# Kernel optimization log

Measured on AMD Instinct MI355X. Metric: run time of the kernel, lower is better.

The kernel has to match this reference:

```python
import jax, jax.numpy as jnp
import numpy as np

BIG = 1.0e6  # sentinel 'infinite' 1D distance (BIG**2 = 1e12 is safely finite in fp32)


def _edt_sq(zero_mask):
    """Exact squared Euclidean distance transform to nearest True in zero_mask.

    Two-pass separable exact EDT (matches scipy.ndimage.distance_transform_edt):
      pass 1: 1-D distance along W via forward/backward cummax scans
      pass 2: min-plus over H: D2[i,j] = min_k g2[k,j] + (i-k)^2
    zero_mask: [H, W] bool (True where the source array equals 0).
    """
    H, W = zero_mask.shape
    col = jnp.arange(W, dtype=jnp.float32)
    # index of last zero to the left / first zero to the right
    last = jax.lax.cummax(jnp.where(zero_mask, col, -BIG), axis=1)
    nxt = -jax.lax.cummax(jnp.where(zero_mask, -col, -BIG), axis=1, reverse=True)
    g = jnp.minimum(jnp.minimum(col - last, nxt - col), BIG)  # [H, W] 1-D dist
    g2 = g * g
    row = jnp.arange(H, dtype=jnp.float32)
    sq = (row[:, None] - row[None, :]) ** 2  # [H, H]
    # D2[i, j] = min_k g2[k, j] + (i - k)^2  -- exact 2-D squared EDT
    return jnp.min(g2[None, :, :] + sq[:, :, None], axis=1)


def _distance_map(mask):
    """Signed distance map: EDT(mask) - EDT(1 - mask); zeros if mask empty."""
    pos = jnp.sqrt(_edt_sq(mask == 0))   # dist of foreground px to nearest background
    neg = jnp.sqrt(_edt_sq(mask != 0))   # dist of background px to nearest foreground
    d = pos - neg
    return jnp.where(mask.sum() == 0, jnp.zeros_like(d), d)


def boundary_loss(pred, target):
    B, C, H, W = pred.shape
    masks = target.reshape(B * C, H, W)
    # sequence over B*C to keep the [H,H,W] min-plus intermediate per-image
    dmaps = jax.lax.map(_distance_map, masks).reshape(B, C, H, W)
    # sum_c mean_{b,h,w}(sig(pred_c)*d_c) / C  ==  overall mean
    return jnp.mean(jax.nn.sigmoid(pred) * dmaps)


def setup_inputs() -> dict:
    key = jax.random.key(0)
    k1, k2 = jax.random.split(key)
    pred = jax.random.normal(k1, (8, 3, 256, 256), dtype=jnp.float32)
    target = jax.random.randint(k2, (8, 3, 256, 256), 0, 2, dtype=jnp.int32)
    return {"pred": pred, "target": target}


def reference(pred, target):
    return boundary_loss(pred, target)
```

## Files before the change

### kernel.cpp

```cpp
#include <hip/hip_runtime.h>
#include <math.h>

#define NIMG 24
#define H    256
#define W    256
#define NPIX (H * W)
#define NROWS (NIMG * H)
#define CPB  16
#define NBLK2 (NIMG * (W / CPB))
#define LDP2 17
#define BIGI 1000000
#define CAPS 1024

__global__ __launch_bounds__(256)
void edt_rows_kernel(const int* __restrict__ tgt,
                     short* __restrict__ f,
                     float* __restrict__ out) {
    if (blockIdx.x == 0 && threadIdx.x == 0) out[0] = 0.0f;

    const int lane = threadIdx.x & 63;
    const int wid  = threadIdx.x >> 6;
    const int gw   = blockIdx.x * 4 + wid;
    const int c0   = lane << 2;

    int4 tvs[4];
#pragma unroll
    for (int s = 0; s < 4; ++s)
        tvs[s] = ((const int4*)(tgt + (((gw << 2) + s) << 8)))[lane];

#pragma unroll
    for (int s = 0; s < 4; ++s) {
        const int row = (gw << 2) + s;
        const int4 tv = tvs[s];

        const int prevw = __shfl_up(tv.w, 1, 64);
        const bool ch0 = (lane > 0) && ((tv.x != 0) != (prevw != 0));
        const bool ch1 = (tv.y != 0) != (tv.x != 0);
        const bool ch2 = (tv.z != 0) != (tv.y != 0);
        const bool ch3 = (tv.w != 0) != (tv.z != 0);

        const int a0 = ch0 ? c0     : -BIGI;
        const int a1 = ch1 ? c0 + 1 : a0;
        const int a2 = ch2 ? c0 + 2 : a1;
        const int a3 = ch3 ? c0 + 3 : a2;
        const int rb3 = ch3 ? c0 + 3 : BIGI;
        const int rb2 = ch2 ? c0 + 2 : rb3;
        const int rb1 = ch1 ? c0 + 1 : rb2;
        const int rb0 = ch0 ? c0     : rb1;

        const unsigned long long mask = __ballot(ch0 | ch1 | ch2 | ch3);
        const unsigned long long lowm = mask & ((1ULL << lane) - 1ULL);
        const unsigned long long him  = (lane < 63) ? (mask >> (lane + 1)) : 0ULL;

        const int plane = 63 - __builtin_clzll(lowm | 1ULL);
        const int sh_a  = __shfl(a3, plane & 63, 64);
        const int ex    = (lowm != 0ULL) ? sh_a : -BIGI;

        const int qlane = lane + 1 +
            (int)__builtin_ctzll(him | 0x8000000000000000ULL);
        const int sh_r  = __shfl(rb0, qlane & 63, 64);
        const int exr   = (him != 0ULL) ? sh_r : BIGI;

        const int s0 = (ex > a0) ? ex : a0;
        const int s1 = (ex > a1) ? ex : a1;
        const int s2 = (ex > a2) ? ex : a2;
        const int s3 = (ex > a3) ? ex : a3;
        const int n0 = (rb1 < exr) ? rb1 : exr;
        const int n1 = (rb2 < exr) ? rb2 : exr;
        const int n2 = (rb3 < exr) ? rb3 : exr;
        const int n3 = exr;

        auto gcalc = [](int c, int ss, int nn) -> int {
            int dp = c - ss + 1;
            int dn = nn - c;
            int g = dp < dn ? dp : dn;
            return (g < BIGI) ? g : CAPS;
        };
        const int g0 = gcalc(c0,     s0, n0);
        const int g1 = gcalc(c0 + 1, s1, n1);
        const int g2 = gcalc(c0 + 2, s2, n2);
        const int g3 = gcalc(c0 + 3, s3, n3);

        short4 o;
        o.x = (short)((tv.x != 0) ? g0 : -g0);
        o.y = (short)((tv.y != 0) ? g1 : -g1);
        o.z = (short)((tv.z != 0) ? g2 : -g2);
        o.w = (short)((tv.w != 0) ? g3 : -g3);
        ((short4*)(f + (row << 8)))[lane] = o;
    }
}

__global__ __launch_bounds__(512)
void edt_cols_kernel(const short* __restrict__ f,
                     const float* __restrict__ pred,
                     float* __restrict__ out) {
    const int bid  = blockIdx.x;
    const int img  = bid >> 4;
    const int j0   = (bid & 15) << 4;
    const int t    = threadIdx.x;
    const int lane = t & 63;
    const int wid  = t >> 6;

    __shared__ float sf[H][LDP2];
    __shared__ double wsum[8];
    __shared__ int nonempty;
    if (t == 0) nonempty = 0;
    __syncthreads();

    {
        const int row = t >> 1;
        const int q   = (t & 1) << 3;
        const int4 rv = *(const int4*)(f + (img << 16) + (row << 8) + j0 + q);
        const short* sv = (const short*)&rv;
        bool ne = false;
#pragma unroll
        for (int j = 0; j < 8; ++j) {
            const int v = sv[j];
            ne = ne || (v != -CAPS);
            float g = (float)v;
            if (v == CAPS)  g =  1.0e6f;
            if (v == -CAPS) g = -1.0e6f;
            sf[row][q + j] = g;
        }
        if (ne) nonempty = 1;
    }

    const int c  = t & 15;
    const int r0 = (t >> 4) << 3;
    float pf[8];
#pragma unroll
    for (int ii = 0; ii < 8; ++ii)
        pf[ii] = pred[(img << 16) + ((r0 + ii) << 8) + j0 + c];

    __syncthreads();
    const int flag = nonempty;

    double acc = 0.0;
#pragma unroll
    for (int ii = 0; ii < 8; ++ii) {
        const int i = r0 + ii;
        const float fv = sf[i][c];
        const bool  m  = fv > 0.0f;
        const float sgn = m ? 1.0f : -1.0f;
        const float gi = fabsf(fv);
        const int  gii = (int)gi;
        int lo = i - gii; lo = lo > 0 ? lo : 0;
        int hi = i + gii; hi = hi < (H - 1) ? hi : (H - 1);

        float dm = 3.0e38f;
        float dk = (float)(i - lo);
        for (int k = lo; k <= hi; ++k) {
            const float g = fmaxf(sgn * sf[k][c], 0.0f);
            dm = fminf(dm, g * g + dk * dk);
            dk -= 1.0f;
        }

        float d = m ? sqrtf(dm) : -sqrtf(dm);
        if (!flag) d = 0.0f;
        const float sig = 1.0f / (1.0f + expf(-pf[ii]));
        acc += (double)sig * (double)d;
    }

#pragma unroll
    for (int off = 32; off > 0; off >>= 1) acc += __shfl_down(acc, off, 64);
    if (lane == 0) wsum[wid] = acc;
    __syncthreads();
    if (t == 0) {
        double s = 0.0;
#pragma unroll
        for (int w = 0; w < 8; ++w) s += wsum[w];
        atomicAdd(out, (float)(s * (1.0 / (double)(NIMG * NPIX))));
    }
}

extern "C" void kernel_launch(void* const* d_in, const int* in_sizes, int n_in,
                              void* d_out, int out_size, void* d_ws, size_t ws_size,
                              hipStream_t stream) {
    const float* pred = (const float*)d_in[0];
    const int*   tgt  = (const int*)d_in[1];
    float* out = (float*)d_out;

    short* fbuf = (short*)d_ws;

    edt_rows_kernel<<<384, 256, 0, stream>>>(tgt, fbuf, out);
    edt_cols_kernel<<<NBLK2, 512, 0, stream>>>(fbuf, pred, out);
}
```

Baseline: 22.83 us.

## Rewrite row EDT pass with 16-pixel-per-thread bitmask scans via shared memory

The row pass previously assigned one wavefront per 4 rows, with 4 pixels per lane, and resolved nearest transitions using ballot and cross-lane shuffles. It now gives each thread 16 contiguous pixels and 16 rows per block. Each thread builds a 16-bit transition mask and publishes it to shared memory, then finds the nearest transitions with clz/ctz over the row's four 64-bit words. This drops the shuffles and gives wider vector loads and stores. In exchange it adds a block barrier, an extra scalar load for the neighbour pixel, and more per-thread serial work.

```diff
diff --git a/kernel.cpp b/kernel.cpp
--- a/kernel.cpp
+++ b/kernel.cpp
@@ -18,76 +18,94 @@
                      float* __restrict__ out) {
     if (blockIdx.x == 0 && threadIdx.x == 0) out[0] = 0.0f;
 
-    const int lane = threadIdx.x & 63;
-    const int wid  = threadIdx.x >> 6;
-    const int gw   = blockIdx.x * 4 + wid;
-    const int c0   = lane << 2;
-
-    int4 tvs[4];
-#pragma unroll
-    for (int s = 0; s < 4; ++s)
-        tvs[s] = ((const int4*)(tgt + (((gw << 2) + s) << 8)))[lane];
-
-#pragma unroll
-    for (int s = 0; s < 4; ++s) {
-        const int row = (gw << 2) + s;
-        const int4 tv = tvs[s];
-
-        const int prevw = __shfl_up(tv.w, 1, 64);
-        const bool ch0 = (lane > 0) && ((tv.x != 0) != (prevw != 0));
-        const bool ch1 = (tv.y != 0) != (tv.x != 0);
-        const bool ch2 = (tv.z != 0) != (tv.y != 0);
-        const bool ch3 = (tv.w != 0) != (tv.z != 0);
-
-        const int a0 = ch0 ? c0     : -BIGI;
-        const int a1 = ch1 ? c0 + 1 : a0;
-        const int a2 = ch2 ? c0 + 2 : a1;
-        const int a3 = ch3 ? c0 + 3 : a2;
-        const int rb3 = ch3 ? c0 + 3 : BIGI;
-        const int rb2 = ch2 ? c0 + 2 : rb3;
-        const int rb1 = ch1 ? c0 + 1 : rb2;
-        const int rb0 = ch0 ? c0     : rb1;
-
-        const unsigned long long mask = __ballot(ch0 | ch1 | ch2 | ch3);
-        const unsigned long long lowm = mask & ((1ULL << lane) - 1ULL);
-        const unsigned long long him  = (lane < 63) ? (mask >> (lane + 1)) : 0ULL;
-
-        const int plane = 63 - __builtin_clzll(lowm | 1ULL);
-        const int sh_a  = __shfl(a3, plane & 63, 64);
-        const int ex    = (lowm != 0ULL) ? sh_a : -BIGI;
-
-        const int qlane = lane + 1 +
-            (int)__builtin_ctzll(him | 0x8000000000000000ULL);
-        const int sh_r  = __shfl(rb0, qlane & 63, 64);
-        const int exr   = (him != 0ULL) ? sh_r : BIGI;
-
-        const int s0 = (ex > a0) ? ex : a0;
-        const int s1 = (ex > a1) ? ex : a1;
-        const int s2 = (ex > a2) ? ex : a2;
-        const int s3 = (ex > a3) ? ex : a3;
-        const int n0 = (rb1 < exr) ? rb1 : exr;
-        const int n1 = (rb2 < exr) ? rb2 : exr;
-        const int n2 = (rb3 < exr) ? rb3 : exr;
-        const int n3 = exr;
-
-        auto gcalc = [](int c, int ss, int nn) -> int {
-            int dp = c - ss + 1;
-            int dn = nn - c;
-            int g = dp < dn ? dp : dn;
-            return (g < BIGI) ? g : CAPS;
-        };
-        const int g0 = gcalc(c0,     s0, n0);
-        const int g1 = gcalc(c0 + 1, s1, n1);
-        const int g2 = gcalc(c0 + 2, s2, n2);
-        const int g3 = gcalc(c0 + 3, s3, n3);
-
-        short4 o;
-        o.x = (short)((tv.x != 0) ? g0 : -g0);
-        o.y = (short)((tv.y != 0) ? g1 : -g1);
-        o.z = (short)((tv.z != 0) ? g2 : -g2);
-        o.w = (short)((tv.w != 0) ? g3 : -g3);
-        ((short4*)(f + (row << 8)))[lane] = o;
-    }
+    const int t    = threadIdx.x;
+    const int rloc = t >> 4;
+    const int ck   = t & 15;
+    const int row  = blockIdx.x * 16 + rloc;
+    const int j0   = ck << 4;
+    const int base = (row << 8) + j0;
+
+    __shared__ unsigned long long m[16][4];
+
+    const int4* rp = (const int4*)(tgt + base);
+    const int4 v0 = rp[0], v1 = rp[1], v2 = rp[2], v3 = rp[3];
+    const int prevv = (ck > 0) ? tgt[base - 1] : 0;
+
+    int va[16];
+    *(int4*)&va[0]  = v0;  *(int4*)&va[4]  = v1;
+    *(int4*)&va[8]  = v2;  *(int4*)&va[12] = v3;
+
+    unsigned int bits = 0;
+    {
+        bool pc = (prevv != 0);
+#pragma unroll
+        for (int i = 0; i < 16; ++i) {
+            const bool c = (va[i] != 0);
+            if (c != pc) bits |= (1u << i);
+            pc = c;
+        }
+        if (ck == 0) bits &= ~1u;
+    }
+    ((unsigned short*)m)[(rloc << 4) + ck] = (unsigned short)bits;
+    __syncthreads();
+
+    const unsigned long long M0 = m[rloc][0], M1 = m[rloc][1];
+    const unsigned long long M2 = m[rloc][2], M3 = m[rloc][3];
+    const int wlo = ck >> 2;
+    const int blo = (ck & 3) << 4;
+    const int bhi = blo + 16;
+
+    const unsigned long long pm  = blo ? ((1ULL << blo) - 1ULL) : 0ULL;
+    const unsigned long long lm0 = (wlo > 0) ? ~0ULL : pm;
+    const unsigned long long lm1 = (wlo > 1) ? ~0ULL : ((wlo == 1) ? pm : 0ULL);
+    const unsigned long long lm2 = (wlo > 2) ? ~0ULL : ((wlo == 2) ? pm : 0ULL);
+    const unsigned long long lm3 = (wlo == 3) ? pm : 0ULL;
+    int last = -BIGI;
+    {
+        unsigned long long x;
+        x = M0 & lm0; if (x) last = 63 - __builtin_clzll(x);
+        x = M1 & lm1; if (x) last = 127 - __builtin_clzll(x);
+        x = M2 & lm2; if (x) last = 191 - __builtin_clzll(x);
+        x = M3 & lm3; if (x) last = 255 - __builtin_clzll(x);
+    }
+
+    const unsigned long long sm  = (bhi == 64) ? 0ULL : ~((1ULL << bhi) - 1ULL);
+    const unsigned long long hm0 = (wlo == 0) ? sm : 0ULL;
+    const unsigned long long hm1 = (wlo < 1) ? ~0ULL : ((wlo == 1) ? sm : 0ULL);
+    const unsigned long long hm2 = (wlo < 2) ? ~0ULL : ((wlo == 2) ? sm : 0ULL);
+    const unsigned long long hm3 = (wlo < 3) ? ~0ULL : sm;
+    int nxt_hi = BIGI;
+    {
+        unsigned long long x;
+        x = M3 & hm3; if (x) nxt_hi = 192 + __builtin_ctzll(x);
+        x = M2 & hm2; if (x) nxt_hi = 128 + __builtin_ctzll(x);
+        x = M1 & hm1; if (x) nxt_hi =  64 + __builtin_ctzll(x);
+        x = M0 & hm0; if (x) nxt_hi =       __builtin_ctzll(x);
+    }
+
+    short os[16];
+    unsigned int rem = bits;
+#pragma unroll
+    for (int i = 0; i < 16; ++i) {
+        const int j = j0 + i;
+        if (rem & 1u) last = j;
+        rem >>= 1;
+        const int n  = rem ? (j + 1 + __builtin_ctz(rem)) : nxt_hi;
+        const int dp = j - last + 1;
+        const int dn = n - j;
+        int g = dp < dn ? dp : dn;
+        g = (g < BIGI) ? g : CAPS;
+        os[i] = (short)((va[i] != 0) ? g : -g);
+    }
+
+    int pk[8];
+#pragma unroll
+    for (int i = 0; i < 8; ++i)
+        pk[i] = (int)((unsigned short)os[2 * i] |
+                      ((unsigned int)(unsigned short)os[2 * i + 1] << 16));
+    int4* op = (int4*)(f + base);
+    op[0] = make_int4(pk[0], pk[1], pk[2], pk[3]);
+    op[1] = make_int4(pk[4], pk[5], pk[6], pk[7]);
 }
 
 __global__ __launch_bounds__(512)
```

Measured after the change: 23.34 us. +2.2%, slower.
